# Kernel optimization log

Measured on AMD Instinct MI355X. Metric: run time of the kernel, lower is better.

Reference implementation:

```python
import jax, jax.numpy as jnp
import numpy as np

N, K, DC, DH = 50000, 32, 64, 64  # nodes, neighbors, dim_c(+dim_h), dim_hidden

def setup_inputs() -> dict:
    key = jax.random.key(0)
    ks = jax.random.split(key, 8)
    return {
        "z":     jax.random.normal(ks[0], (N, DC), dtype=jnp.float32),
        "z_":    jax.random.normal(ks[1], (N, K, DC), dtype=jnp.float32),
        "W_cur": jax.random.normal(ks[2], (DC, DH), dtype=jnp.float32) * 0.1,
        "b_cur": jax.random.uniform(ks[3], (DH,), minval=-0.1, maxval=0.1, dtype=jnp.float32),
        "W_nbr": jax.random.normal(ks[4], (2 * DC, DH), dtype=jnp.float32) * 0.1,
        "b_nbr": jax.random.uniform(ks[5], (DH,), minval=-0.1, maxval=0.1, dtype=jnp.float32),
        "W_out": jax.random.normal(ks[6], (2 * DH, DC), dtype=jnp.float32) * 0.1,
        "b_out": jax.random.uniform(ks[7], (DC,), minval=-0.1, maxval=0.1, dtype=jnp.float32),
    }

def reference(z, z_, W_cur, b_cur, W_nbr, b_nbr, W_out, b_out):
    # cur branch: CELU(Linear(z))  -> [N, DH]
    v = jax.nn.celu(z @ W_cur + b_cur)
    # nbr branch: concat(self expanded over nbr axis, neighbors) -> [N, K, 2*DC]
    zz = jnp.concatenate((jnp.broadcast_to(z[:, None, :], z_.shape), z_), axis=-1)
    # CELU(Linear) then sum over neighbor axis -> [N, DH]
    v_ = jax.nn.celu(zz @ W_nbr + b_nbr).sum(axis=-2)
    # final linear on concatenated features -> [N, DC]
    dc = jnp.concatenate((v, v_), axis=-1) @ W_out + b_out
    return dc
```

## Files before the change

### kernel.cpp

```cpp
#include <hip/hip_runtime.h>
#include <hip/hip_bf16.h>

typedef float  f32x16 __attribute__((ext_vector_type(16)));
typedef short  bf16x8 __attribute__((ext_vector_type(8)));

__device__ __forceinline__ unsigned short f2bf(float x) {
  union { float f; unsigned u; } v; v.f = x;
  return (unsigned short)((v.u + 0x7FFFu + ((v.u >> 16) & 1u)) >> 16);
}
__device__ __forceinline__ float bf2f(unsigned short u) {
  union { unsigned u; float f; } v; v.u = ((unsigned)u) << 16; return v.f;
}
__device__ __forceinline__ float celu1(float x) {
  return x > 0.f ? x : (__expf(x) - 1.f);
}

struct Stage { float4 a[4][2]; };

__device__ __forceinline__ void issue_stage(Stage& s, const float* __restrict__ aptr,
                                            int lo, int hi) {
#pragma unroll
  for (int ks = 0; ks < 4; ++ks) {
    const float* pa = aptr + lo * 64 + ks * 16 + 8 * hi;
    s.a[ks][0] = *reinterpret_cast<const float4*>(pa);
    s.a[ks][1] = *reinterpret_cast<const float4*>(pa + 4);
  }
}

__device__ __forceinline__ bf16x8 to_frag(float4 a, float4 b) {
  bf16x8 r;
  r[0] = (short)f2bf(a.x); r[1] = (short)f2bf(a.y);
  r[2] = (short)f2bf(a.z); r[3] = (short)f2bf(a.w);
  r[4] = (short)f2bf(b.x); r[5] = (short)f2bf(b.y);
  r[6] = (short)f2bf(b.z); r[7] = (short)f2bf(b.w);
  return r;
}

__device__ __forceinline__ bf16x8 ldsfrag(const unsigned short* w, int S, int col, int k0) {
  return *reinterpret_cast<const bf16x8*>(w + col * S + (k0 ^ ((col & 7) << 3)));
}

__device__ __forceinline__ bf16x8 wfrag(const float* __restrict__ W, int ld, int col, int k0) {
  bf16x8 f;
#pragma unroll
  for (int j = 0; j < 8; ++j) f[j] = (short)f2bf(W[(size_t)(k0 + j) * ld + col]);
  return f;
}

__global__ __launch_bounds__(256, 2) void gcu_kernel(
    const float* __restrict__ z, const float* __restrict__ z_,
    const float* __restrict__ Wc, const float* __restrict__ bc,
    const float* __restrict__ Wn, const float* __restrict__ bn,
    const float* __restrict__ Wo, const float* __restrict__ bo,
    float* __restrict__ out, int N) {
  __shared__ __align__(16) unsigned short sWnT[64 * 128];
  __shared__ __align__(16) unsigned short sVV[4][32 * 128];
  __shared__ __align__(16) unsigned short sT[4][32 * 64];

  const int tid = threadIdx.x;
  const int wid = tid >> 6, lane = tid & 63;
  const int lo = lane & 31, hi = lane >> 5;

  for (int i = tid; i < 128 * 64; i += 256) {
    int c = i & 63, k = i >> 6;
    sWnT[c * 128 + (k ^ ((c & 7) << 3))] = f2bf(Wn[i]);
  }
  __syncthreads();

  const int task = blockIdx.x + (int)gridDim.x * wid;
  const int base = task * 32;
  if (base >= N) return;

  unsigned short* vv = &sVV[wid][0];
  unsigned short* tt = &sT[wid][0];

  {
    int r = lane >> 1, seg = lane & 1;
    int node = min(base + r, N - 1);
    const float* src = z + (size_t)node * 64 + seg * 32;
    int m = (r & 7) << 3;
#pragma unroll
    for (int q = 0; q < 4; ++q) {
      float4 x0 = *reinterpret_cast<const float4*>(src + q * 8);
      float4 x1 = *reinterpret_cast<const float4*>(src + q * 8 + 4);
      *reinterpret_cast<bf16x8*>(vv + r * 128 + ((seg * 32 + q * 8) ^ m)) = to_frag(x0, x1);
    }
  }

  const float bn0 = bn[lo], bn1 = bn[32 + lo];
  const float bc0 = bc[lo], bc1 = bc[32 + lo];
  const float bo0 = bo[lo], bo1 = bo[32 + lo];

  {
    f32x16 a0{}, a1{};
#pragma unroll
    for (int ks = 0; ks < 4; ++ks) {
      int k0 = ks * 16 + 8 * hi;
      bf16x8 af = *reinterpret_cast<const bf16x8*>(vv + lo * 128 + (k0 ^ ((lo & 7) << 3)));
      bf16x8 b0 = ldsfrag(sWnT, 128, lo, k0);
      bf16x8 b1 = ldsfrag(sWnT, 128, lo + 32, k0);
      a0 = __builtin_amdgcn_mfma_f32_32x32x16_bf16(af, b0, a0, 0, 0, 0);
      a1 = __builtin_amdgcn_mfma_f32_32x32x16_bf16(af, b1, a1, 0, 0, 0);
    }
#pragma unroll
    for (int r = 0; r < 16; ++r) {
      int row = (r & 3) + 8 * (r >> 2) + 4 * hi;
      tt[row * 64 + lo]      = f2bf(a0[r]);
      tt[row * 64 + 32 + lo] = f2bf(a1[r]);
    }
  }

  bf16x8 Bn[4][2];
#pragma unroll
  for (int ks = 0; ks < 4; ++ks) {
    int k0 = 64 + ks * 16 + 8 * hi;
    Bn[ks][0] = ldsfrag(sWnT, 128, lo, k0);
    Bn[ks][1] = ldsfrag(sWnT, 128, lo + 32, k0);
  }

  auto aptr_of = [&](int n) { return z_ + (size_t)min(base + n, N - 1) * 2048; };

  auto process = [&](const Stage& s, int n) {
    float c0 = bn0 + bf2f(tt[n * 64 + lo]);
    float c1 = bn1 + bf2f(tt[n * 64 + 32 + lo]);
    f32x16 acc0{}, acc1{};
#pragma unroll
    for (int ks = 0; ks < 4; ++ks) {
      bf16x8 af = to_frag(s.a[ks][0], s.a[ks][1]);
      acc0 = __builtin_amdgcn_mfma_f32_32x32x16_bf16(af, Bn[ks][0], acc0, 0, 0, 0);
      acc1 = __builtin_amdgcn_mfma_f32_32x32x16_bf16(af, Bn[ks][1], acc1, 0, 0, 0);
    }
    float s0 = 0.f, s1 = 0.f;
#pragma unroll
    for (int r = 0; r < 16; ++r) {
      s0 += celu1(acc0[r] + c0);
      s1 += celu1(acc1[r] + c1);
    }
    s0 += __shfl_xor(s0, 32, 64);
    s1 += __shfl_xor(s1, 32, 64);
    if (hi == 0) {
      vv[n * 128 + ((64 + lo) ^ ((n & 7) << 3))] = f2bf(s0);
      vv[n * 128 + ((96 + lo) ^ ((n & 7) << 3))] = f2bf(s1);
    }
  };

  Stage sA, sB;
  issue_stage(sA, aptr_of(0), lo, hi);
#pragma unroll 1
  for (int nn = 0; nn < 32; nn += 2) {
    issue_stage(sB, aptr_of(nn + 1), lo, hi);
    process(sA, nn);
    issue_stage(sA, aptr_of(nn + 2), lo, hi);
    process(sB, nn + 1);
  }

  {
    f32x16 a0{}, a1{};
#pragma unroll
    for (int ks = 0; ks < 4; ++ks) {
      int k0 = ks * 16 + 8 * hi;
      bf16x8 af = *reinterpret_cast<const bf16x8*>(vv + lo * 128 + (k0 ^ ((lo & 7) << 3)));
      bf16x8 b0 = wfrag(Wc, 64, lo, k0);
      bf16x8 b1 = wfrag(Wc, 64, lo + 32, k0);
      a0 = __builtin_amdgcn_mfma_f32_32x32x16_bf16(af, b0, a0, 0, 0, 0);
      a1 = __builtin_amdgcn_mfma_f32_32x32x16_bf16(af, b1, a1, 0, 0, 0);
    }
#pragma unroll
    for (int r = 0; r < 16; ++r) {
      int row = (r & 3) + 8 * (r >> 2) + 4 * hi;
      vv[row * 128 + ( lo       ^ ((row & 7) << 3))] = f2bf(celu1(a0[r] + bc0));
      vv[row * 128 + ((32 + lo) ^ ((row & 7) << 3))] = f2bf(celu1(a1[r] + bc1));
    }
  }

  {
    f32x16 a0{}, a1{};
#pragma unroll
    for (int ks = 0; ks < 8; ++ks) {
      int k0 = ks * 16 + 8 * hi;
      bf16x8 af = *reinterpret_cast<const bf16x8*>(vv + lo * 128 + (k0 ^ ((lo & 7) << 3)));
      bf16x8 b0 = wfrag(Wo, 64, lo, k0);
      bf16x8 b1 = wfrag(Wo, 64, lo + 32, k0);
      a0 = __builtin_amdgcn_mfma_f32_32x32x16_bf16(af, b0, a0, 0, 0, 0);
      a1 = __builtin_amdgcn_mfma_f32_32x32x16_bf16(af, b1, a1, 0, 0, 0);
    }
#pragma unroll
    for (int r = 0; r < 16; ++r) {
      int row = base + (r & 3) + 8 * (r >> 2) + 4 * hi;
      if (row < N) {
        out[(size_t)row * 64 + lo]      = a0[r] + bo0;
        out[(size_t)row * 64 + 32 + lo] = a1[r] + bo1;
      }
    }
  }
}

extern "C" void kernel_launch(void* const* d_in, const int* in_sizes, int n_in,
                              void* d_out, int out_size, void* d_ws, size_t ws_size,
                              hipStream_t stream) {
  const float* z  = (const float*)d_in[0];
  const float* z_ = (const float*)d_in[1];
  const float* Wc = (const float*)d_in[2];
  const float* bc = (const float*)d_in[3];
  const float* Wn = (const float*)d_in[4];
  const float* bn = (const float*)d_in[5];
  const float* Wo = (const float*)d_in[6];
  const float* bo = (const float*)d_in[7];
  float* out = (float*)d_out;
  const int N = in_sizes[0] / 64;
  const int tasks = (N + 31) / 32;
  int blocks = 512;
  while (blocks * 4 < tasks) blocks += 256;
  gcu_kernel<<<blocks, 256, 0, stream>>>(z, z_, Wc, bc, Wn, bn, Wo, bo, out, N);
}
```

Before: 99.19 us.

## Stream neighbor tiles into LDS via global_load_lds and keep z fragments in registers

Replaces the register double-buffered global loads of each node's 32x64 neighbor tile with direct global-to-LDS async copies (global_load_lds) into a per-wave swizzled fp32 tile, then reads fragments from LDS. The z fragments are loaded once into registers and reused for both the z@Wn and z@Wc products, and the shared-memory layout is split into separate buffers. The intent is to cut VGPR pressure and improve memory-level parallelism. The trade-off is that each iteration waits for vmcnt(0), giving only single-stage prefetch with a full wait per node. It also uses more LDS, which may lower occupancy.

```diff
diff --git a/kernel.cpp b/kernel.cpp
--- a/kernel.cpp
+++ b/kernel.cpp
@@ -13,18 +13,6 @@
 }
 __device__ __forceinline__ float celu1(float x) {
   return x > 0.f ? x : (__expf(x) - 1.f);
-}
-
-struct Stage { float4 a[4][2]; };
-
-__device__ __forceinline__ void issue_stage(Stage& s, const float* __restrict__ aptr,
-                                            int lo, int hi) {
-#pragma unroll
-  for (int ks = 0; ks < 4; ++ks) {
-    const float* pa = aptr + lo * 64 + ks * 16 + 8 * hi;
-    s.a[ks][0] = *reinterpret_cast<const float4*>(pa);
-    s.a[ks][1] = *reinterpret_cast<const float4*>(pa + 4);
-  }
 }
 
 __device__ __forceinline__ bf16x8 to_frag(float4 a, float4 b) {
@@ -54,8 +42,9 @@
     const float* __restrict__ Wo, const float* __restrict__ bo,
     float* __restrict__ out, int N) {
   __shared__ __align__(16) unsigned short sWnT[64 * 128];
-  __shared__ __align__(16) unsigned short sVV[4][32 * 128];
   __shared__ __align__(16) unsigned short sT[4][32 * 64];
+  __shared__ __align__(16) unsigned short sV[4][32 * 64];
+  __shared__ __align__(16) float sTile[4][32 * 64];
 
   const int tid = threadIdx.x;
   const int wid = tid >> 6, lane = tid & 63;
@@ -71,36 +60,52 @@
   const int base = task * 32;
   if (base >= N) return;
 
-  unsigned short* vv = &sVV[wid][0];
   unsigned short* tt = &sT[wid][0];
-
-  {
-    int r = lane >> 1, seg = lane & 1;
-    int node = min(base + r, N - 1);
-    const float* src = z + (size_t)node * 64 + seg * 32;
-    int m = (r & 7) << 3;
-#pragma unroll
-    for (int q = 0; q < 4; ++q) {
-      float4 x0 = *reinterpret_cast<const float4*>(src + q * 8);
-      float4 x1 = *reinterpret_cast<const float4*>(src + q * 8 + 4);
-      *reinterpret_cast<bf16x8*>(vv + r * 128 + ((seg * 32 + q * 8) ^ m)) = to_frag(x0, x1);
-    }
-  }
+  unsigned short* sv = &sV[wid][0];
+  float* tile = &sTile[wid][0];
+
+  const int rl = lane >> 4, tl = lane & 15;
+  const int o0 = rl * 64 + ((tl ^ rl) << 2);
+  const int o1 = o0 ^ 16;
+
+  auto stage_tile = [&](const float* gb) {
+#pragma unroll
+    for (int i = 0; i < 8; ++i) {
+      const float* src = gb + i * 256 + ((i & 1) ? o1 : o0);
+      __builtin_amdgcn_global_load_lds(
+          (const __attribute__((address_space(1))) unsigned*)src,
+          (__attribute__((address_space(3))) unsigned*)(tile + i * 256),
+          16, 0, 0);
+    }
+  };
+
+  stage_tile(z_ + (size_t)base * 2048);
 
   const float bn0 = bn[lo], bn1 = bn[32 + lo];
   const float bc0 = bc[lo], bc1 = bc[32 + lo];
   const float bo0 = bo[lo], bo1 = bo[32 + lo];
 
+  bf16x8 zf[4];
+  {
+    int node = min(base + lo, N - 1);
+    const float* zp = z + (size_t)node * 64;
+#pragma unroll
+    for (int ks = 0; ks < 4; ++ks) {
+      float4 x0 = *reinterpret_cast<const float4*>(zp + ks * 16 + 8 * hi);
+      float4 x1 = *reinterpret_cast<const float4*>(zp + ks * 16 + 8 * hi + 4);
+      zf[ks] = to_frag(x0, x1);
+    }
+  }
+
   {
     f32x16 a0{}, a1{};
 #pragma unroll
     for (int ks = 0; ks < 4; ++ks) {
       int k0 = ks * 16 + 8 * hi;
-      bf16x8 af = *reinterpret_cast<const bf16x8*>(vv + lo * 128 + (k0 ^ ((lo & 7) << 3)));
       bf16x8 b0 = ldsfrag(sWnT, 128, lo, k0);
       bf16x8 b1 = ldsfrag(sWnT, 128, lo + 32, k0);
-      a0 = __builtin_amdgcn_mfma_f32_32x32x16_bf16(af, b0, a0, 0, 0, 0);
-      a1 = __builtin_amdgcn_mfma_f32_32x32x16_bf16(af, b1, a1, 0, 0, 0);
+      a0 = __builtin_amdgcn_mfma_f32_32x32x16_bf16(zf[ks], b0, a0, 0, 0, 0);
+      a1 = __builtin_amdgcn_mfma_f32_32x32x16_bf16(zf[ks], b1, a1, 0, 0, 0);
     }
 #pragma unroll
     for (int r = 0; r < 16; ++r) {
@@ -110,25 +115,43 @@
     }
   }
 
-  bf16x8 Bn[4][2];
+  bf16x8 Bn_[4][2];
 #pragma unroll
   for (int ks = 0; ks < 4; ++ks) {
     int k0 = 64 + ks * 16 + 8 * hi;
-    Bn[ks][0] = ldsfrag(sWnT, 128, lo, k0);
-    Bn[ks][1] = ldsfrag(sWnT, 128, lo + 32, k0);
-  }
-
-  auto aptr_of = [&](int n) { return z_ + (size_t)min(base + n, N - 1) * 2048; };
-
-  auto process = [&](const Stage& s, int n) {
-    float c0 = bn0 + bf2f(tt[n * 64 + lo]);
-    float c1 = bn1 + bf2f(tt[n * 64 + 32 + lo]);
+    Bn_[ks][0] = ldsfrag(sWnT, 128, lo, k0);
+    Bn_[ks][1] = ldsfrag(sWnT, 128, lo + 32, k0);
+  }
+
+  int roff[8];
+#pragma unroll
+  for (int ks = 0; ks < 4; ++ks)
+#pragma unroll
+    for (int p = 0; p < 2; ++p)
+      roff[ks * 2 + p] = lo * 256 + (((ks * 4 + 2 * hi + p) ^ (lo & 7)) << 4);
+  const char* tb = (const char*)tile;
+
+#pragma unroll 1
+  for (int nn = 0; nn < 32; ++nn) {
+    asm volatile("s_waitcnt vmcnt(0)" ::: "memory");
+    __builtin_amdgcn_sched_barrier(0);
+    float4 q[8];
+#pragma unroll
+    for (int j = 0; j < 8; ++j) q[j] = *reinterpret_cast<const float4*>(tb + roff[j]);
+    bf16x8 af[4];
+#pragma unroll
+    for (int ks = 0; ks < 4; ++ks) af[ks] = to_frag(q[2 * ks], q[2 * ks + 1]);
+    asm volatile("s_waitcnt lgkmcnt(0)" ::: "memory");
+    __builtin_amdgcn_sched_barrier(0);
+    if (nn < 31) stage_tile(z_ + (size_t)min(base + nn + 1, N - 1) * 2048);
+
+    float c0 = bn0 + bf2f(tt[nn * 64 + lo]);
+    float c1 = bn1 + bf2f(tt[nn * 64 + 32 + lo]);
     f32x16 acc0{}, acc1{};
 #pragma unroll
     for (int ks = 0; ks < 4; ++ks) {
-      bf16x8 af = to_frag(s.a[ks][0], s.a[ks][1]);
-      acc0 = __builtin_amdgcn_mfma_f32_32x32x16_bf16(af, Bn[ks][0], acc0, 0, 0, 0);
-      acc1 = __builtin_amdgcn_mfma_f32_32x32x16_bf16(af, Bn[ks][1], acc1, 0, 0, 0);
+      acc0 = __builtin_amdgcn_mfma_f32_32x32x16_bf16(af[ks], Bn_[ks][0], acc0, 0, 0, 0);
+      acc1 = __builtin_amdgcn_mfma_f32_32x32x16_bf16(af[ks], Bn_[ks][1], acc1, 0, 0, 0);
     }
     float s0 = 0.f, s1 = 0.f;
 #pragma unroll
@@ -139,50 +162,41 @@
     s0 += __shfl_xor(s0, 32, 64);
     s1 += __shfl_xor(s1, 32, 64);
     if (hi == 0) {
-      vv[n * 128 + ((64 + lo) ^ ((n & 7) << 3))] = f2bf(s0);
-      vv[n * 128 + ((96 + lo) ^ ((n & 7) << 3))] = f2bf(s1);
-    }
-  };
-
-  Stage sA, sB;
-  issue_stage(sA, aptr_of(0), lo, hi);
-#pragma unroll 1
-  for (int nn = 0; nn < 32; nn += 2) {
-    issue_stage(sB, aptr_of(nn + 1), lo, hi);
-    process(sA, nn);
-    issue_stage(sA, aptr_of(nn + 2), lo, hi);
-    process(sB, nn + 1);
-  }
-
+      int m = (nn & 7) << 3;
+      sv[nn * 64 + ( lo       ^ m)] = f2bf(s0);
+      sv[nn * 64 + ((32 + lo) ^ m)] = f2bf(s1);
+    }
+  }
+
+  unsigned short* vt = (unsigned short*)tile;
   {
     f32x16 a0{}, a1{};
 #pragma unroll
     for (int ks = 0; ks < 4; ++ks) {
       int k0 = ks * 16 + 8 * hi;
-      bf16x8 af = *reinterpret_cast<const bf16x8*>(vv + lo * 128 + (k0 ^ ((lo & 7) << 3)));
-      bf16x8 b0 = wfrag(Wc, 64, lo, k0);
-      bf16x8 b1 = wfrag(Wc, 64, lo + 32, k0);
-      a0 = __builtin_amdgcn_mfma_f32_32x32x16_bf16(af, b0, a0, 0, 0, 0);
-      a1 = __builtin_amdgcn_mfma_f32_32x32x16_bf16(af, b1, a1, 0, 0, 0);
+      a0 = __builtin_amdgcn_mfma_f32_32x32x16_bf16(zf[ks], wfrag(Wc, 64, lo, k0), a0, 0, 0, 0);
+      a1 = __builtin_amdgcn_mfma_f32_32x32x16_bf16(zf[ks], wfrag(Wc, 64, lo + 32, k0), a1, 0, 0, 0);
     }
 #pragma unroll
     for (int r = 0; r < 16; ++r) {
       int row = (r & 3) + 8 * (r >> 2) + 4 * hi;
-      vv[row * 128 + ( lo       ^ ((row & 7) << 3))] = f2bf(celu1(a0[r] + bc0));
-      vv[row * 128 + ((32 + lo) ^ ((row & 7) << 3))] = f2bf(celu1(a1[r] + bc1));
+      int m = (row & 7) << 3;
+      vt[row * 64 + ( lo       ^ m)] = f2bf(celu1(a0[r] + bc0));
+      vt[row * 64 + ((32 + lo) ^ m)] = f2bf(celu1(a1[r] + bc1));
     }
   }
 
   {
     f32x16 a0{}, a1{};
+    const int mm = (lo & 7) << 3;
 #pragma unroll
     for (int ks = 0; ks < 8; ++ks) {
       int k0 = ks * 16 + 8 * hi;
-      bf16x8 af = *reinterpret_cast<const bf16x8*>(vv + lo * 128 + (k0 ^ ((lo & 7) << 3)));
-      bf16x8 b0 = wfrag(Wo, 64, lo, k0);
-      bf16x8 b1 = wfrag(Wo, 64, lo + 32, k0);
-      a0 = __builtin_amdgcn_mfma_f32_32x32x16_bf16(af, b0, a0, 0, 0, 0);
-      a1 = __builtin_amdgcn_mfma_f32_32x32x16_bf16(af, b1, a1, 0, 0, 0);
+      bf16x8 af;
+      if (ks < 4) af = *reinterpret_cast<const bf16x8*>(vt + lo * 64 + ( k0        ^ mm));
+      else        af = *reinterpret_cast<const bf16x8*>(sv + lo * 64 + ((k0 - 64)  ^ mm));
+      a0 = __builtin_amdgcn_mfma_f32_32x32x16_bf16(af, wfrag(Wo, 64, lo, k0), a0, 0, 0, 0);
+      a1 = __builtin_amdgcn_mfma_f32_32x32x16_bf16(af, wfrag(Wo, 64, lo + 32, k0), a1, 0, 0, 0);
     }
 #pragma unroll
     for (int r = 0; r < 16; ++r) {
```

Result: faster. 96.51 us (-2.7%).
